# Kernel tuning notes

Hardware: AMD Instinct MI355X
Metric: run time of the kernel (lower is better)

Reference implementation:

```python
import jax, jax.numpy as jnp
import numpy as np

DIM = 1024
NUM_HEADS = 16
HEAD_D = DIM // NUM_HEADS


def setup_inputs() -> dict:
    key = jax.random.key(0)
    ks = jax.random.split(key, 9)
    B, T, D = 4, 2048, DIM
    s = 1.0 / np.sqrt(D)
    return {
        "x": jax.random.normal(ks[0], (B, T, D), dtype=jnp.float32),
        "Wq": jax.random.normal(ks[1], (D, D), dtype=jnp.float32) * s,
        "bq": jnp.zeros((D,), dtype=jnp.float32),
        "Wk": jax.random.normal(ks[2], (D, D), dtype=jnp.float32) * s,
        "bk": jnp.zeros((D,), dtype=jnp.float32),
        "Wv": jax.random.normal(ks[3], (D, D), dtype=jnp.float32) * s,
        "bv": jnp.zeros((D,), dtype=jnp.float32),
        "Wo": jax.random.normal(ks[4], (D, D), dtype=jnp.float32) * s,
        "bo": jnp.zeros((D,), dtype=jnp.float32),
    }


def reference(x, Wq, bq, Wk, bk, Wv, bv, Wo, bo):
    B, T, D = x.shape
    H, Hd = NUM_HEADS, HEAD_D
    # QKV projections (torch Linear: x @ W.T + b)
    q = (x @ Wq.T + bq).reshape(B, T, H, Hd).transpose(0, 2, 1, 3)  # [B,H,T,Hd]
    k = (x @ Wk.T + bk).reshape(B, T, H, Hd).transpose(0, 2, 1, 3)
    v = (x @ Wv.T + bv).reshape(B, T, H, Hd).transpose(0, 2, 1, 3)
    scores = jnp.einsum("bhqd,bhkd->bhqk", q, k) / jnp.sqrt(jnp.float32(Hd))
    probs = jax.nn.softmax(scores, axis=-1)
    out = jnp.einsum("bhqk,bhkd->bhqd", probs, v)  # [B,H,T,Hd]
    out = out.transpose(0, 2, 1, 3).reshape(B, T, D)
    return out @ Wo.T + bo
```

## Files before the change

### kernel.cpp

```cpp
#include <hip/hip_runtime.h>

typedef unsigned short u16;
typedef unsigned int   u32;
typedef __bf16 bf16;
typedef __attribute__((ext_vector_type(8))) __bf16 bf16x8;
typedef __attribute__((ext_vector_type(4))) float  f32x4;


__device__ __forceinline__ u16 f2bf(float f) {
  u32 u = __float_as_uint(f);
  u32 r = (u + 0x7fffu + ((u >> 16) & 1u)) >> 16;
  return (u16)r;
}

__device__ __forceinline__ void gload_lds16(const void* g, void* l) {
  __builtin_amdgcn_global_load_lds((__attribute__((address_space(1))) u32*)g,
                                   (__attribute__((address_space(3))) u32*)l,
                                   16, 0, 0);
}

__device__ __forceinline__ u32 cvt_pk_bf16(float lo, float hi) {
  u32 r;
  asm("v_cvt_pk_bf16_f32 %0, %1, %2" : "=v"(r) : "v"(lo), "v"(hi));
  return r;
}

#define SCL_LOG2E 0.1803368801111204f


__global__ __launch_bounds__(256) void cvt_bf16_kernel(const float* __restrict__ in,
                                                       u16* __restrict__ out, int n4) {
  int i = blockIdx.x * blockDim.x + threadIdx.x;
  int stride = gridDim.x * blockDim.x;
  for (; i < n4; i += stride) {
    float4 v = ((const float4*)in)[i];
    uint2 o;
    o.x = (u32)f2bf(v.x) | ((u32)f2bf(v.y) << 16);
    o.y = (u32)f2bf(v.z) | ((u32)f2bf(v.w) << 16);
    ((uint2*)out)[i] = o;
  }
}

__global__ __launch_bounds__(256) void cvt4_kernel(const float* __restrict__ p0,
                                                   const float* __restrict__ p1,
                                                   const float* __restrict__ p2,
                                                   const float* __restrict__ p3,
                                                   u16* o0, u16* o1, u16* o2, u16* o3) {
  const int which = blockIdx.x >> 8;
  const float* in = which == 0 ? p0 : which == 1 ? p1 : which == 2 ? p2 : p3;
  u16* out = which == 0 ? o0 : which == 1 ? o1 : which == 2 ? o2 : o3;
  int i = (blockIdx.x & 255) * 256 + threadIdx.x;
  #pragma unroll
  for (int r = 0; r < 4; ++r, i += 65536) {
    float4 v = ((const float4*)in)[i];
    uint2 o;
    o.x = (u32)f2bf(v.x) | ((u32)f2bf(v.y) << 16);
    o.y = (u32)f2bf(v.z) | ((u32)f2bf(v.w) << 16);
    ((uint2*)out)[i] = o;
  }
}


#define GK 1024
#define GN 1024

__global__ __launch_bounds__(256) void gemm_qkv_kernel(const u16* __restrict__ A,
                                                       const u16* __restrict__ Wq,
                                                       const u16* __restrict__ Wk,
                                                       const u16* __restrict__ Wv,
                                                       const float* __restrict__ bq,
                                                       const float* __restrict__ bk,
                                                       const float* __restrict__ bv,
                                                       u16* __restrict__ Qo,
                                                       u16* __restrict__ Ko,
                                                       u16* __restrict__ Vo) {
  __shared__ u16 sA[2][128 * 32];
  __shared__ u16 sB[2][128 * 32];

  const int tid  = threadIdx.x;
  const int lane = tid & 63;
  const int w    = tid >> 6;
  const int wm   = w >> 1, wn = w & 1;
  const int lid  = (blockIdx.x & 7) * 192 + (blockIdx.x >> 3);
  const int which = lid >> 9;
  const int sub   = lid & 511;
  const u16*  W    = which == 0 ? Wq : which == 1 ? Wk : Wv;
  const float* bias = which == 0 ? bq : which == 1 ? bk : bv;
  const int tn   = sub & 7;
  const int tm   = sub >> 3;
  const int m0   = tm * 128, n0 = tn * 128;
  const int rgrp = lane >> 4, rlo = lane & 15;

  const int c0 = (w * 2 + 0) * 64 + lane;
  const int c1 = (w * 2 + 1) * 64 + lane;
  const int r0 = c0 >> 2, col0 = (((c0 & 3) ^ (r0 & 3)) * 8);
  const int r1 = c1 >> 2, col1 = (((c1 & 3) ^ (r1 & 3)) * 8);
  const u16* aS0 = A + (size_t)(m0 + r0) * GK + col0;
  const u16* aS1 = A + (size_t)(m0 + r1) * GK + col1;
  const u16* bS0 = W + (size_t)(n0 + r0) * GK + col0;
  const u16* bS1 = W + (size_t)(n0 + r1) * GK + col1;

  auto stage = [&](u16* dA, u16* dB, int kt) {
    int k0 = kt * 32;
    gload_lds16(aS0 + k0, dA + (w * 2 + 0) * 512);
    gload_lds16(aS1 + k0, dA + (w * 2 + 1) * 512);
    gload_lds16(bS0 + k0, dB + (w * 2 + 0) * 512);
    gload_lds16(bS1 + k0, dB + (w * 2 + 1) * 512);
  };

  f32x4 acc[4][4] = {};

  auto compute = [&](const u16* sAc, const u16* sBc) {
    bf16x8 a[4], b[4];
    #pragma unroll
    for (int i = 0; i < 4; ++i) {
      int row = wm * 64 + i * 16 + rlo;
      int cb  = rgrp ^ (row & 3);
      a[i] = *(const bf16x8*)&sAc[row * 32 + cb * 8];
    }
    #pragma unroll
    for (int j = 0; j < 4; ++j) {
      int row = wn * 64 + j * 16 + rlo;
      int cb  = rgrp ^ (row & 3);
      b[j] = *(const bf16x8*)&sBc[row * 32 + cb * 8];
    }
    #pragma unroll
    for (int i = 0; i < 4; ++i)
      #pragma unroll
      for (int j = 0; j < 4; ++j)
        acc[i][j] = __builtin_amdgcn_mfma_f32_16x16x32_bf16(a[i], b[j], acc[i][j], 0, 0, 0);
  };

  stage(sA[0], sB[0], 0);
  __syncthreads();

  for (int kt = 0; kt < GK / 32; kt += 2) {
    stage(sA[1], sB[1], kt + 1);
    compute(sA[0], sB[0]);
    __syncthreads();
    if (kt + 2 < GK / 32) stage(sA[0], sB[0], kt + 2);
    compute(sA[1], sB[1]);
    __syncthreads();
  }

  if (which <= 1) {
    u16* out = which == 0 ? Qo : Ko;
    const float scl = which == 0 ? 1.0f : SCL_LOG2E;
    #pragma unroll
    for (int i = 0; i < 4; ++i)
      #pragma unroll
      for (int j = 0; j < 4; ++j)
        #pragma unroll
        for (int r = 0; r < 4; ++r) {
          int m = m0 + wm * 64 + i * 16 + rgrp * 4 + r;
          int n = n0 + wn * 64 + j * 16 + rlo;
          float v = (acc[i][j][r] + bias[n]) * scl;
          out[(size_t)m * GN + n] = (u16)__builtin_bit_cast(u16, (bf16)v);
        }
  } else {
    #pragma unroll
    for (int i = 0; i < 4; ++i)
      #pragma unroll
      for (int j = 0; j < 4; ++j) {
        int mb = m0 + wm * 64 + i * 16 + rgrp * 4;
        int n  = n0 + wn * 64 + j * 16 + rlo;
        int b = mb >> 11, t = mb & 2047, h = n >> 6, hd = n & 63;
        float bv_ = bias[n];
        uint2 st;
        st.x = cvt_pk_bf16(acc[i][j][0] + bv_, acc[i][j][1] + bv_);
        st.y = cvt_pk_bf16(acc[i][j][2] + bv_, acc[i][j][3] + bv_);
        *(uint2*)&Vo[((size_t)(b * 16 + h) * 64 + hd) * 2048 + t] = st;
      }
  }
}

__global__ __launch_bounds__(256) void gemm_out_kernel(const u16* __restrict__ A,
                                                       const u16* __restrict__ W,
                                                       const float* __restrict__ bias,
                                                       float* __restrict__ Cout) {
  __shared__ u16 sA[2][128 * 32];
  __shared__ u16 sB[2][128 * 32];

  const int tid  = threadIdx.x;
  const int lane = tid & 63;
  const int w    = tid >> 6;
  const int wm   = w >> 1, wn = w & 1;
  const int lid  = (blockIdx.x & 7) * 64 + (blockIdx.x >> 3);
  const int tn   = lid & 7;
  const int tm   = lid >> 3;
  const int m0   = tm * 128, n0 = tn * 128;
  const int rgrp = lane >> 4, rlo = lane & 15;

  const int c0 = (w * 2 + 0) * 64 + lane;
  const int c1 = (w * 2 + 1) * 64 + lane;
  const int r0 = c0 >> 2, col0 = (((c0 & 3) ^ (r0 & 3)) * 8);
  const int r1 = c1 >> 2, col1 = (((c1 & 3) ^ (r1 & 3)) * 8);
  const u16* aS0 = A + (size_t)(m0 + r0) * GK + col0;
  const u16* aS1 = A + (size_t)(m0 + r1) * GK + col1;
  const u16* bS0 = W + (size_t)(n0 + r0) * GK + col0;
  const u16* bS1 = W + (size_t)(n0 + r1) * GK + col1;

  auto stage = [&](u16* dA, u16* dB, int kt) {
    int k0 = kt * 32;
    gload_lds16(aS0 + k0, dA + (w * 2 + 0) * 512);
    gload_lds16(aS1 + k0, dA + (w * 2 + 1) * 512);
    gload_lds16(bS0 + k0, dB + (w * 2 + 0) * 512);
    gload_lds16(bS1 + k0, dB + (w * 2 + 1) * 512);
  };

  f32x4 acc[4][4] = {};

  auto compute = [&](const u16* sAc, const u16* sBc) {
    bf16x8 a[4], b[4];
    #pragma unroll
    for (int i = 0; i < 4; ++i) {
      int row = wm * 64 + i * 16 + rlo;
      int cb  = rgrp ^ (row & 3);
      a[i] = *(const bf16x8*)&sAc[row * 32 + cb * 8];
    }
    #pragma unroll
    for (int j = 0; j < 4; ++j) {
      int row = wn * 64 + j * 16 + rlo;
      int cb  = rgrp ^ (row & 3);
      b[j] = *(const bf16x8*)&sBc[row * 32 + cb * 8];
    }
    #pragma unroll
    for (int i = 0; i < 4; ++i)
      #pragma unroll
      for (int j = 0; j < 4; ++j)
        acc[i][j] = __builtin_amdgcn_mfma_f32_16x16x32_bf16(a[i], b[j], acc[i][j], 0, 0, 0);
  };

  stage(sA[0], sB[0], 0);
  __syncthreads();

  for (int kt = 0; kt < GK / 32; kt += 2) {
    stage(sA[1], sB[1], kt + 1);
    compute(sA[0], sB[0]);
    __syncthreads();
    if (kt + 2 < GK / 32) stage(sA[0], sB[0], kt + 2);
    compute(sA[1], sB[1]);
    __syncthreads();
  }

  #pragma unroll
  for (int i = 0; i < 4; ++i)
    #pragma unroll
    for (int j = 0; j < 4; ++j)
      #pragma unroll
      for (int r = 0; r < 4; ++r) {
        int m = m0 + wm * 64 + i * 16 + rgrp * 4 + r;
        int n = n0 + wn * 64 + j * 16 + rlo;
        Cout[(size_t)m * GN + n] = acc[i][j][r] + bias[n];
      }
}


__global__ __launch_bounds__(256) void attn_kernel(const u16* __restrict__ Q,
                                                   const u16* __restrict__ K,
                                                   const u16* __restrict__ Vt,
                                                   bf16* __restrict__ O) {
  __shared__ u16 sK[2][64 * 64];
  __shared__ u16 sV[2][64 * 64];

  const int tid  = threadIdx.x;
  const int lane = tid & 63;
  const int w    = tid >> 6;
  const int rgrp = lane >> 4, rlo = lane & 15;
  const int bid  = (blockIdx.x & 7) * 128 + (blockIdx.x >> 3);
  const int qt   = bid & 15;
  const int bh   = bid >> 4;
  const int b    = bh >> 4, h = bh & 15;

  const u16* Qh = Q  + (size_t)b * 2048 * 1024 + h * 64;
  const u16* Kh = K  + (size_t)b * 2048 * 1024 + h * 64;
  const u16* Vh = Vt + (size_t)bh * 64 * 2048;

  const int c0 = (w * 2 + 0) * 64 + lane;
  const int c1 = (w * 2 + 1) * 64 + lane;
  const int r0 = c0 >> 3, col0 = ((c0 & 7) ^ (r0 & 7)) * 8;
  const int r1 = c1 >> 3, col1 = ((c1 & 7) ^ (r1 & 7)) * 8;
  const u16* kb0 = Kh + (size_t)r0 * 1024 + col0;
  const u16* kb1 = Kh + (size_t)r1 * 1024 + col1;
  const u16* vb0 = Vh + (size_t)r0 * 2048 + col0;
  const u16* vb1 = Vh + (size_t)r1 * 2048 + col1;

  auto stage = [&](u16* dK, u16* dV) {
    gload_lds16(kb0, dK + (w * 2 + 0) * 512);
    gload_lds16(kb1, dK + (w * 2 + 1) * 512);
    gload_lds16(vb0, dV + (w * 2 + 0) * 512);
    gload_lds16(vb1, dV + (w * 2 + 1) * 512);
    kb0 += 65536; kb1 += 65536;
    vb0 += 64;    vb1 += 64;
  };

  stage(sK[0], sV[0]);

  bf16x8 bQ[2][2];
  #pragma unroll
  for (int qg = 0; qg < 2; ++qg) {
    int q0 = qt * 128 + w * 32 + qg * 16 + rlo;
    bQ[qg][0] = *(const bf16x8*)&Qh[(size_t)q0 * 1024 + rgrp * 8];
    bQ[qg][1] = *(const bf16x8*)&Qh[(size_t)q0 * 1024 + 32 + rgrp * 8];
  }

  bf16x8 vones;
  #pragma unroll
  for (int i = 0; i < 8; ++i) vones[i] = (bf16)1.0f;
  const f32x4 FZ = {0.f, 0.f, 0.f, 0.f};

  asm volatile("s_waitcnt vmcnt(0)" ::: "memory");
  __builtin_amdgcn_s_barrier();
  __builtin_amdgcn_sched_barrier(0);

  f32x4 lden[2] = {};
  f32x4 o[2][4] = {};
  f32x4 sT[2][4];

  auto qk = [&](const u16* sKc) {
    __builtin_amdgcn_s_setprio(1);
    #pragma unroll
    for (int nt = 0; nt < 4; ++nt) {
      int row = nt * 16 + rlo;
      int cb0_ = (0 + rgrp) ^ (row & 7);
      int cb1_ = (4 + rgrp) ^ (row & 7);
      bf16x8 aK0 = *(const bf16x8*)&sKc[row * 64 + cb0_ * 8];
      bf16x8 aK1 = *(const bf16x8*)&sKc[row * 64 + cb1_ * 8];
      sT[0][nt] = __builtin_amdgcn_mfma_f32_16x16x32_bf16(aK0, bQ[0][0], FZ, 0, 0, 0);
      sT[1][nt] = __builtin_amdgcn_mfma_f32_16x16x32_bf16(aK0, bQ[1][0], FZ, 0, 0, 0);
      sT[0][nt] = __builtin_amdgcn_mfma_f32_16x16x32_bf16(aK1, bQ[0][1], sT[0][nt], 0, 0, 0);
      sT[1][nt] = __builtin_amdgcn_mfma_f32_16x16x32_bf16(aK1, bQ[1][1], sT[1][nt], 0, 0, 0);
    }
    __builtin_amdgcn_s_setprio(0);
  };

  auto smpv = [&](const u16* sVc) {
    #pragma unroll
    for (int qg = 0; qg < 2; ++qg) {
      #pragma unroll
      for (int nt = 0; nt < 4; ++nt)
        #pragma unroll
        for (int r = 0; r < 4; ++r)
          sT[qg][nt][r] = __builtin_amdgcn_exp2f(sT[qg][nt][r]);

      u32 pw[4][2];
      #pragma unroll
      for (int nt = 0; nt < 4; ++nt) {
        pw[nt][0] = cvt_pk_bf16(sT[qg][nt][0], sT[qg][nt][1]);
        pw[nt][1] = cvt_pk_bf16(sT[qg][nt][2], sT[qg][nt][3]);
      }
      bf16x8 bP[2];
      #pragma unroll
      for (int kk = 0; kk < 2; ++kk) {
        u32 a0 = pw[2 * kk][0], b0 = pw[2 * kk + 1][0];
        u32 a1 = pw[2 * kk][1], b1 = pw[2 * kk + 1][1];
        asm("v_permlane32_swap_b32 %0, %1" : "+v"(a0), "+v"(b0));
        asm("v_permlane16_swap_b32 %0, %1" : "+v"(a0), "+v"(b0));
        asm("v_permlane32_swap_b32 %0, %1" : "+v"(a1), "+v"(b1));
        asm("v_permlane16_swap_b32 %0, %1" : "+v"(a1), "+v"(b1));
        union { u32 u[4]; bf16x8 v; } fu;
        fu.u[0] = a0; fu.u[1] = a1; fu.u[2] = b0; fu.u[3] = b1;
        bP[kk] = fu.v;
      }

      __builtin_amdgcn_s_setprio(1);
      #pragma unroll
      for (int kk = 0; kk < 2; ++kk) {
        lden[qg] = __builtin_amdgcn_mfma_f32_16x16x32_bf16(vones, bP[kk], lden[qg], 0, 0, 0);
        #pragma unroll
        for (int dt = 0; dt < 4; ++dt) {
          int rowv = dt * 16 + rlo;
          int cbv  = (kk * 4 + rgrp) ^ (rowv & 7);
          bf16x8 aV = *(const bf16x8*)&sVc[rowv * 64 + cbv * 8];
          o[qg][dt] = __builtin_amdgcn_mfma_f32_16x16x32_bf16(aV, bP[kk], o[qg][dt], 0, 0, 0);
        }
      }
      __builtin_amdgcn_s_setprio(0);
    }
  };

  auto iter = [&](const u16* sKc, const u16* sVc, u16* sKn, u16* sVn) {
    stage(sKn, sVn);
    qk(sKc);
    asm volatile("s_waitcnt vmcnt(4)" ::: "memory");
    __builtin_amdgcn_s_barrier();
    __builtin_amdgcn_sched_barrier(0);
    smpv(sVc);
    asm volatile("s_waitcnt vmcnt(2)" ::: "memory");
    __builtin_amdgcn_s_barrier();
    __builtin_amdgcn_sched_barrier(0);
  };

  for (int it = 0; it < 15; ++it) {
    iter(sK[0], sV[0], sK[1], sV[1]);
    iter(sK[1], sV[1], sK[0], sV[0]);
  }
  iter(sK[0], sV[0], sK[1], sV[1]);

  qk(sK[1]);
  asm volatile("s_waitcnt vmcnt(0)" ::: "memory");
  __builtin_amdgcn_s_barrier();
  __builtin_amdgcn_sched_barrier(0);
  smpv(sV[1]);

  #pragma unroll
  for (int qg = 0; qg < 2; ++qg) {
    const float inv = 1.0f / lden[qg][0];
    const int tq = qt * 128 + w * 32 + qg * 16 + rlo;
    #pragma unroll
    for (int dt = 0; dt < 4; ++dt) {
      uint2 st;
      st.x = cvt_pk_bf16(o[qg][dt][0] * inv, o[qg][dt][1] * inv);
      st.y = cvt_pk_bf16(o[qg][dt][2] * inv, o[qg][dt][3] * inv);
      *(uint2*)&O[((size_t)(b * 2048 + tq)) * 1024 + h * 64 + dt * 16 + rgrp * 4] = st;
    }
  }
}


extern "C" void kernel_launch(void* const* d_in, const int* in_sizes, int n_in,
                              void* d_out, int out_size, void* d_ws, size_t ws_size,
                              hipStream_t stream) {
  const float* x  = (const float*)d_in[0];
  const float* Wq = (const float*)d_in[1];
  const float* bq = (const float*)d_in[2];
  const float* Wk = (const float*)d_in[3];
  const float* bk = (const float*)d_in[4];
  const float* Wv = (const float*)d_in[5];
  const float* bv = (const float*)d_in[6];
  const float* Wo = (const float*)d_in[7];
  const float* bo = (const float*)d_in[8];

  char* ws = (char*)d_ws;
  u16* xb  = (u16*)(ws);
  u16* Wqb = (u16*)(ws + 16777216);
  u16* Wkb = (u16*)(ws + 18874368);
  u16* Wvb = (u16*)(ws + 20971520);
  u16* Wob = (u16*)(ws + 23068672);
  u16* Qb  = (u16*)(ws + 25165824);
  u16* Kb  = (u16*)(ws + 41943040);
  u16* Vtb = (u16*)(ws + 58720256);
  u16* Ab  = (u16*)(ws + 75497472);

  cvt_bf16_kernel<<<4096, 256, 0, stream>>>(x, xb, 8388608 / 4);
  cvt4_kernel<<<1024, 256, 0, stream>>>(Wq, Wk, Wv, Wo, Wqb, Wkb, Wvb, Wob);

  gemm_qkv_kernel<<<1536, 256, 0, stream>>>(xb, Wqb, Wkb, Wvb, bq, bk, bv, Qb, Kb, Vtb);

  attn_kernel<<<1024, 256, 0, stream>>>(Qb, Kb, Vtb, (bf16*)Ab);

  gemm_out_kernel<<<512, 256, 0, stream>>>(Ab, Wob, bo, (float*)d_out);
}
```

Measured before the change: 213.3 us.

## Deepen GEMM LDS pipeline to four stages with vmcnt-based waits

Both projection GEMMs move from a double-buffered LDS pipeline with __syncthreads to a four-buffer ring. Three tiles are prefetched ahead, and each step waits only on outstanding global-to-LDS loads via s_waitcnt vmcnt plus a raw s_barrier. The aim is to hide global memory latency better and cut full barrier waits. In exchange, LDS use per block doubles to 64KB, which may reduce occupancy, and correctness now depends on the hand-set vmcnt counts.

Measured after the change: 220.5 us. 3.4% more time.

```diff
diff --git a/kernel.cpp b/kernel.cpp
--- a/kernel.cpp
+++ b/kernel.cpp
@@ -64,6 +64,81 @@
 #define GK 1024
 #define GN 1024
 
+#define GEMM_PRELUDE                                                            \
+  const int tid  = threadIdx.x;                                                 \
+  const int lane = tid & 63;                                                    \
+  const int w    = tid >> 6;                                                    \
+  const int wm   = w >> 1, wn = w & 1;                                          \
+  const int rgrp = lane >> 4, rlo = lane & 15;                                  \
+  const int c0 = (w * 2 + 0) * 64 + lane;                                       \
+  const int c1 = (w * 2 + 1) * 64 + lane;                                       \
+  const int r0 = c0 >> 2, col0 = (((c0 & 3) ^ (r0 & 3)) * 8);                   \
+  const int r1 = c1 >> 2, col1 = (((c1 & 3) ^ (r1 & 3)) * 8);                   \
+  const u16* aS0 = A + (size_t)(m0 + r0) * GK + col0;                           \
+  const u16* aS1 = A + (size_t)(m0 + r1) * GK + col1;                           \
+  const u16* bS0 = W + (size_t)(n0 + r0) * GK + col0;                           \
+  const u16* bS1 = W + (size_t)(n0 + r1) * GK + col1;                           \
+  auto stage = [&](u16* dA, u16* dB) {                                          \
+    gload_lds16(aS0, dA + (w * 2 + 0) * 512);                                   \
+    gload_lds16(aS1, dA + (w * 2 + 1) * 512);                                   \
+    gload_lds16(bS0, dB + (w * 2 + 0) * 512);                                   \
+    gload_lds16(bS1, dB + (w * 2 + 1) * 512);                                   \
+    aS0 += 32; aS1 += 32; bS0 += 32; bS1 += 32;                                 \
+  };                                                                            \
+  f32x4 acc[4][4] = {};                                                         \
+  auto compute = [&](const u16* sAc, const u16* sBc) {                          \
+    bf16x8 a[4], b[4];                                                          \
+    _Pragma("unroll")                                                           \
+    for (int i = 0; i < 4; ++i) {                                               \
+      int row = wm * 64 + i * 16 + rlo;                                         \
+      int cb  = rgrp ^ (row & 3);                                               \
+      a[i] = *(const bf16x8*)&sAc[row * 32 + cb * 8];                           \
+    }                                                                           \
+    _Pragma("unroll")                                                           \
+    for (int j = 0; j < 4; ++j) {                                               \
+      int row = wn * 64 + j * 16 + rlo;                                         \
+      int cb  = rgrp ^ (row & 3);                                               \
+      b[j] = *(const bf16x8*)&sBc[row * 32 + cb * 8];                           \
+    }                                                                           \
+    _Pragma("unroll")                                                           \
+    for (int i = 0; i < 4; ++i)                                                 \
+      _Pragma("unroll")                                                         \
+      for (int j = 0; j < 4; ++j)                                               \
+        acc[i][j] = __builtin_amdgcn_mfma_f32_16x16x32_bf16(a[i], b[j],         \
+                                                            acc[i][j], 0, 0, 0);\
+  };                                                                            \
+                        \
+  stage(sA[0], sB[0]); stage(sA[1], sB[1]); stage(sA[2], sB[2]);                \
+                 \
+  for (int t = 0; t < 28; t += 4) {                                             \
+    asm volatile("s_waitcnt vmcnt(8)" ::: "memory");                            \
+    __builtin_amdgcn_s_barrier(); __builtin_amdgcn_sched_barrier(0);            \
+    stage(sA[3], sB[3]); compute(sA[0], sB[0]);                                 \
+    asm volatile("s_waitcnt vmcnt(8)" ::: "memory");                            \
+    __builtin_amdgcn_s_barrier(); __builtin_amdgcn_sched_barrier(0);            \
+    stage(sA[0], sB[0]); compute(sA[1], sB[1]);                                 \
+    asm volatile("s_waitcnt vmcnt(8)" ::: "memory");                            \
+    __builtin_amdgcn_s_barrier(); __builtin_amdgcn_sched_barrier(0);            \
+    stage(sA[1], sB[1]); compute(sA[2], sB[2]);                                 \
+    asm volatile("s_waitcnt vmcnt(8)" ::: "memory");                            \
+    __builtin_amdgcn_s_barrier(); __builtin_amdgcn_sched_barrier(0);            \
+    stage(sA[2], sB[2]); compute(sA[3], sB[3]);                                 \
+  }                                                                             \
+                                             \
+  asm volatile("s_waitcnt vmcnt(8)" ::: "memory");                              \
+  __builtin_amdgcn_s_barrier(); __builtin_amdgcn_sched_barrier(0);              \
+  stage(sA[3], sB[3]); compute(sA[0], sB[0]);                                   \
+                                                       \
+  asm volatile("s_waitcnt vmcnt(8)" ::: "memory");                              \
+  __builtin_amdgcn_s_barrier(); __builtin_amdgcn_sched_barrier(0);              \
+  compute(sA[1], sB[1]);                                                        \
+  asm volatile("s_waitcnt vmcnt(4)" ::: "memory");                              \
+  __builtin_amdgcn_s_barrier(); __builtin_amdgcn_sched_barrier(0);              \
+  compute(sA[2], sB[2]);                                                        \
+  asm volatile("s_waitcnt vmcnt(0)" ::: "memory");                              \
+  __builtin_amdgcn_s_barrier(); __builtin_amdgcn_sched_barrier(0);              \
+  compute(sA[3], sB[3]);
+
 __global__ __launch_bounds__(256) void gemm_qkv_kernel(const u16* __restrict__ A,
                                                        const u16* __restrict__ Wq,
                                                        const u16* __restrict__ Wk,
@@ -74,13 +149,9 @@
                                                        u16* __restrict__ Qo,
                                                        u16* __restrict__ Ko,
                                                        u16* __restrict__ Vo) {
-  __shared__ u16 sA[2][128 * 32];
-  __shared__ u16 sB[2][128 * 32];
-
-  const int tid  = threadIdx.x;
-  const int lane = tid & 63;
-  const int w    = tid >> 6;
-  const int wm   = w >> 1, wn = w & 1;
+  __shared__ u16 sA[4][128 * 32];
+  __shared__ u16 sB[4][128 * 32];
+
   const int lid  = (blockIdx.x & 7) * 192 + (blockIdx.x >> 3);
   const int which = lid >> 9;
   const int sub   = lid & 511;
@@ -89,59 +160,8 @@
   const int tn   = sub & 7;
   const int tm   = sub >> 3;
   const int m0   = tm * 128, n0 = tn * 128;
-  const int rgrp = lane >> 4, rlo = lane & 15;
-
-  const int c0 = (w * 2 + 0) * 64 + lane;
-  const int c1 = (w * 2 + 1) * 64 + lane;
-  const int r0 = c0 >> 2, col0 = (((c0 & 3) ^ (r0 & 3)) * 8);
-  const int r1 = c1 >> 2, col1 = (((c1 & 3) ^ (r1 & 3)) * 8);
-  const u16* aS0 = A + (size_t)(m0 + r0) * GK + col0;
-  const u16* aS1 = A + (size_t)(m0 + r1) * GK + col1;
-  const u16* bS0 = W + (size_t)(n0 + r0) * GK + col0;
-  const u16* bS1 = W + (size_t)(n0 + r1) * GK + col1;
-
-  auto stage = [&](u16* dA, u16* dB, int kt) {
-    int k0 = kt * 32;
-    gload_lds16(aS0 + k0, dA + (w * 2 + 0) * 512);
-    gload_lds16(aS1 + k0, dA + (w * 2 + 1) * 512);
-    gload_lds16(bS0 + k0, dB + (w * 2 + 0) * 512);
-    gload_lds16(bS1 + k0, dB + (w * 2 + 1) * 512);
-  };
-
-  f32x4 acc[4][4] = {};
-
-  auto compute = [&](const u16* sAc, const u16* sBc) {
-    bf16x8 a[4], b[4];
-    #pragma unroll
-    for (int i = 0; i < 4; ++i) {
-      int row = wm * 64 + i * 16 + rlo;
-      int cb  = rgrp ^ (row & 3);
-      a[i] = *(const bf16x8*)&sAc[row * 32 + cb * 8];
-    }
-    #pragma unroll
-    for (int j = 0; j < 4; ++j) {
-      int row = wn * 64 + j * 16 + rlo;
-      int cb  = rgrp ^ (row & 3);
-      b[j] = *(const bf16x8*)&sBc[row * 32 + cb * 8];
-    }
-    #pragma unroll
-    for (int i = 0; i < 4; ++i)
-      #pragma unroll
-      for (int j = 0; j < 4; ++j)
-        acc[i][j] = __builtin_amdgcn_mfma_f32_16x16x32_bf16(a[i], b[j], acc[i][j], 0, 0, 0);
-  };
-
-  stage(sA[0], sB[0], 0);
-  __syncthreads();
-
-  for (int kt = 0; kt < GK / 32; kt += 2) {
-    stage(sA[1], sB[1], kt + 1);
-    compute(sA[0], sB[0]);
-    __syncthreads();
-    if (kt + 2 < GK / 32) stage(sA[0], sB[0], kt + 2);
-    compute(sA[1], sB[1]);
-    __syncthreads();
-  }
+
+  GEMM_PRELUDE
 
   if (which <= 1) {
     u16* out = which == 0 ? Qo : Ko;
@@ -178,70 +198,15 @@
                                                        const u16* __restrict__ W,
                                                        const float* __restrict__ bias,
                                                        float* __restrict__ Cout) {
-  __shared__ u16 sA[2][128 * 32];
-  __shared__ u16 sB[2][128 * 32];
-
-  const int tid  = threadIdx.x;
-  const int lane = tid & 63;
-  const int w    = tid >> 6;
-  const int wm   = w >> 1, wn = w & 1;
+  __shared__ u16 sA[4][128 * 32];
+  __shared__ u16 sB[4][128 * 32];
+
   const int lid  = (blockIdx.x & 7) * 64 + (blockIdx.x >> 3);
   const int tn   = lid & 7;
   const int tm   = lid >> 3;
   const int m0   = tm * 128, n0 = tn * 128;
-  const int rgrp = lane >> 4, rlo = lane & 15;
-
-  const int c0 = (w * 2 + 0) * 64 + lane;
-  const int c1 = (w * 2 + 1) * 64 + lane;
-  const int r0 = c0 >> 2, col0 = (((c0 & 3) ^ (r0 & 3)) * 8);
-  const int r1 = c1 >> 2, col1 = (((c1 & 3) ^ (r1 & 3)) * 8);
-  const u16* aS0 = A + (size_t)(m0 + r0) * GK + col0;
-  const u16* aS1 = A + (size_t)(m0 + r1) * GK + col1;
-  const u16* bS0 = W + (size_t)(n0 + r0) * GK + col0;
-  const u16* bS1 = W + (size_t)(n0 + r1) * GK + col1;
-
-  auto stage = [&](u16* dA, u16* dB, int kt) {
-    int k0 = kt * 32;
-    gload_lds16(aS0 + k0, dA + (w * 2 + 0) * 512);
-    gload_lds16(aS1 + k0, dA + (w * 2 + 1) * 512);
-    gload_lds16(bS0 + k0, dB + (w * 2 + 0) * 512);
-    gload_lds16(bS1 + k0, dB + (w * 2 + 1) * 512);
-  };
-
-  f32x4 acc[4][4] = {};
-
-  auto compute = [&](const u16* sAc, const u16* sBc) {
-    bf16x8 a[4], b[4];
-    #pragma unroll
-    for (int i = 0; i < 4; ++i) {
-      int row = wm * 64 + i * 16 + rlo;
-      int cb  = rgrp ^ (row & 3);
-      a[i] = *(const bf16x8*)&sAc[row * 32 + cb * 8];
-    }
-    #pragma unroll
-    for (int j = 0; j < 4; ++j) {
-      int row = wn * 64 + j * 16 + rlo;
-      int cb  = rgrp ^ (row & 3);
-      b[j] = *(const bf16x8*)&sBc[row * 32 + cb * 8];
-    }
-    #pragma unroll
-    for (int i = 0; i < 4; ++i)
-      #pragma unroll
-      for (int j = 0; j < 4; ++j)
-        acc[i][j] = __builtin_amdgcn_mfma_f32_16x16x32_bf16(a[i], b[j], acc[i][j], 0, 0, 0);
-  };
-
-  stage(sA[0], sB[0], 0);
-  __syncthreads();
-
-  for (int kt = 0; kt < GK / 32; kt += 2) {
-    stage(sA[1], sB[1], kt + 1);
-    compute(sA[0], sB[0]);
-    __syncthreads();
-    if (kt + 2 < GK / 32) stage(sA[0], sB[0], kt + 2);
-    compute(sA[1], sB[1]);
-    __syncthreads();
-  }
+
+  GEMM_PRELUDE
 
   #pragma unroll
   for (int i = 0; i < 4; ++i)
```
